# Kernel tuning notes

Measured on AMD Instinct MI355X. Metric: run time of the kernel, lower is better.

Reference implementation:

```python
import jax, jax.numpy as jnp
import numpy as np

B, S, D = 64, 2048, 512

def setup_inputs() -> dict:
    key = jax.random.key(0)
    k1, k2, k3, k4, k5 = jax.random.split(key, 5)
    x = jax.random.normal(k1, (B, S, D), dtype=jnp.float32)
    # torch Linear(dim, dim): weight [D, D], bias [D]
    W1 = jax.random.normal(k2, (D, D), dtype=jnp.float32) * (1.0 / np.sqrt(D))
    b1 = jax.random.normal(k3, (D,), dtype=jnp.float32) * 0.01
    # torch Linear(dim, 1): weight [1, D] -> stored as [D], bias scalar
    w2 = jax.random.normal(k4, (D,), dtype=jnp.float32) * (1.0 / np.sqrt(D))
    b2 = jax.random.normal(k5, (), dtype=jnp.float32) * 0.01
    return {"x": x, "W1": W1, "b1": b1, "w2": w2, "b2": b2}

def reference(x, W1, b1, w2, b2):
    # score MLP: Linear -> Tanh -> Linear(->1), squeeze
    h = jnp.tanh(jnp.einsum('bsd,ed->bse', x, W1) + b1)   # [B,S,D]
    scores = jnp.einsum('bsd,d->bs', h, w2) + b2          # [B,S]
    w = jax.nn.softmax(scores, axis=1)[..., None]         # [B,S,1]
    ctx = jnp.sum(x * w, axis=1)                          # [B,D]
    return (ctx, w)
```

## Files before the change

### kernel.cpp

```cpp
#include <hip/hip_runtime.h>
#include <hip/hip_bf16.h>

#define BB 64
#define SS 2048
#define DD 512
#define MTOT (BB * SS)

typedef __attribute__((ext_vector_type(8))) short short8;
typedef __attribute__((ext_vector_type(8))) unsigned short ushort8;
typedef __attribute__((ext_vector_type(4))) float f32x4;

__device__ __forceinline__ unsigned short f2bf(float f){
  union { float f; unsigned int u; } a; a.f = f;
  unsigned int r = a.u + 0x7fffu + ((a.u >> 16) & 1u);
  return (unsigned short)(r >> 16);
}

__device__ __forceinline__ ushort8 pack8(float4 a, float4 b){
  ushort8 u;
  u[0]=f2bf(a.x); u[1]=f2bf(a.y); u[2]=f2bf(a.z); u[3]=f2bf(a.w);
  u[4]=f2bf(b.x); u[5]=f2bf(b.y); u[6]=f2bf(b.z); u[7]=f2bf(b.w);
  return u;
}

__device__ __forceinline__ void gload_lds16(const unsigned short* g, unsigned short* l){
  __builtin_amdgcn_global_load_lds(
      (const __attribute__((address_space(1))) unsigned int*)g,
      (__attribute__((address_space(3))) unsigned int*)l, 16, 0, 0);
}

__global__ void cvt_w1_kernel(const float* __restrict__ W1, unsigned short* __restrict__ W1s){
  int i = blockIdx.x * blockDim.x + threadIdx.x;
  int s  = i >> 11;
  int g  = i & 2047;
  int kc = g >> 9;
  int e  = (g & 511) ^ kc;
  const float* src = W1 + (size_t)e * DD + s * 32 + kc * 8;
  float4 f0 = *(const float4*)src;
  float4 f1 = *(const float4*)(src + 4);
  *(ushort8*)(W1s + (size_t)i * 8) = pack8(f0, f1);
}

__launch_bounds__(512, 4)
__global__ void scores_kernel(const float* __restrict__ x,
                              const unsigned short* __restrict__ W1s,
                              const float* __restrict__ b1,
                              const float* __restrict__ w2,
                              float* __restrict__ scorep){
  __shared__ __align__(16) unsigned short lds[2][18432];

  const int t    = threadIdx.x;
  const int lane = t & 63;
  const int wid  = t >> 6;
  const int m0   = blockIdx.x * 64;
  const int arow = lane & 15;
  const int kgrp = lane >> 4;

  f32x4 acc[4][4];
  #pragma unroll
  for (int mt = 0; mt < 4; ++mt)
    #pragma unroll
    for (int et = 0; et < 4; ++et)
      acc[mt][et] = (f32x4){0.f, 0.f, 0.f, 0.f};

  const int srow = t >> 2;
  const int skc  = t & 3;
  const float* asrc0 = x + (size_t)(m0 + srow) * DD + skc * 8;
  const int awoff = ((skc << 6) + (srow ^ skc)) << 4;

  const unsigned short* bsrc0 = W1s + ((size_t)((wid << 2) << 6) + lane) * 8;

  #pragma unroll
  for (int j = 0; j < 4; ++j)
    gload_lds16(bsrc0 + j * 512, &lds[0][2048 + ((wid << 2) + j) * 512]);
  if (t < 256){
    float4 f0 = *(const float4*)asrc0;
    float4 f1 = *(const float4*)(asrc0 + 4);
    *(ushort8*)((char*)&lds[0][0] + awoff) = pack8(f0, f1);
  }
  __syncthreads();

  for (int s = 0; s < 16; ++s){
    unsigned short* cur = &lds[s & 1][0];
    unsigned short* nxt = &lds[(s + 1) & 1][0];

    float4 f0, f1;
    if (s < 15){
      const unsigned short* bs = bsrc0 + (size_t)(s + 1) * 16384;
      #pragma unroll
      for (int j = 0; j < 4; ++j)
        gload_lds16(bs + j * 512, nxt + 2048 + ((wid << 2) + j) * 512);
      if (t < 256){
        const float* as = asrc0 + (s + 1) * 32;
        f0 = *(const float4*)as;
        f1 = *(const float4*)(as + 4);
      }
    }

    short8 af[4], bf[4];
    #pragma unroll
    for (int mt = 0; mt < 4; ++mt){
      int row = mt * 16 + arow;
      af[mt] = *(const short8*)((char*)cur + (((kgrp << 6) + (row ^ kgrp)) << 4));
    }
    #pragma unroll
    for (int et = 0; et < 4; ++et){
      int e = (wid << 6) + (et << 4) + arow;
      bf[et] = *(const short8*)((char*)cur + 4096 + (((kgrp << 9) + (e ^ kgrp)) << 4));
    }

    __builtin_amdgcn_s_setprio(1);
    #pragma unroll
    for (int mt = 0; mt < 4; ++mt)
      #pragma unroll
      for (int et = 0; et < 4; ++et)
        acc[mt][et] = __builtin_amdgcn_mfma_f32_16x16x32_bf16(af[mt], bf[et], acc[mt][et], 0, 0, 0);
    __builtin_amdgcn_s_setprio(0);

    if (s < 15 && t < 256)
      *(ushort8*)((char*)nxt + awoff) = pack8(f0, f1);

    __syncthreads();
  }

  float ps[4][4];
  #pragma unroll
  for (int mt = 0; mt < 4; ++mt)
    #pragma unroll
    for (int i = 0; i < 4; ++i) ps[mt][i] = 0.f;

  #pragma unroll
  for (int et = 0; et < 4; ++et){
    int e = (wid << 6) + (et << 4) + arow;
    float b1v = b1[e];
    float w2v = w2[e];
    #pragma unroll
    for (int mt = 0; mt < 4; ++mt){
      #pragma unroll
      for (int i = 0; i < 4; ++i){
        float g = acc[mt][et][i] + b1v;
        g = fminf(15.f, fmaxf(-15.f, g));
        float ex = __expf(2.f * g);
        ps[mt][i] += (1.f - 2.f / (ex + 1.f)) * w2v;
      }
    }
  }
  #pragma unroll
  for (int mt = 0; mt < 4; ++mt)
    #pragma unroll
    for (int i = 0; i < 4; ++i){
      float v = ps[mt][i];
      v += __shfl_xor(v, 1);
      v += __shfl_xor(v, 2);
      v += __shfl_xor(v, 4);
      v += __shfl_xor(v, 8);
      ps[mt][i] = v;
    }
  float* psum = (float*)&lds[0][0];
  if ((lane & 15) == 0){
    #pragma unroll
    for (int mt = 0; mt < 4; ++mt)
      #pragma unroll
      for (int i = 0; i < 4; ++i)
        psum[wid * 64 + mt * 16 + (lane >> 4) * 4 + i] = ps[mt][i];
  }
  __syncthreads();
  if (t < 64){
    float ssum = 0.f;
    #pragma unroll
    for (int w = 0; w < 8; ++w) ssum += psum[w * 64 + t];
    scorep[m0 + t] = ssum;
  }
}

__global__ void softmax_kernel(const float* __restrict__ scorep, float* __restrict__ wout){
  const int b = blockIdx.x;
  const int t = threadIdx.x;
  float v[8];
  #pragma unroll
  for (int i = 0; i < 8; ++i) v[i] = scorep[(size_t)b * SS + t + i * 256];
  float m = v[0];
  #pragma unroll
  for (int i = 1; i < 8; ++i) m = fmaxf(m, v[i]);
  #pragma unroll
  for (int msk = 32; msk >= 1; msk >>= 1) m = fmaxf(m, __shfl_xor(m, msk));
  __shared__ float redm[4], reds[4];
  if ((t & 63) == 0) redm[t >> 6] = m;
  __syncthreads();
  m = fmaxf(fmaxf(redm[0], redm[1]), fmaxf(redm[2], redm[3]));
  float s = 0.f;
  #pragma unroll
  for (int i = 0; i < 8; ++i){ v[i] = __expf(v[i] - m); s += v[i]; }
  #pragma unroll
  for (int msk = 32; msk >= 1; msk >>= 1) s += __shfl_xor(s, msk);
  if ((t & 63) == 0) reds[t >> 6] = s;
  __syncthreads();
  s = reds[0] + reds[1] + reds[2] + reds[3];
  float inv = 1.f / s;
  #pragma unroll
  for (int i = 0; i < 8; ++i) wout[(size_t)b * SS + t + i * 256] = v[i] * inv;
}

__global__ void ctx_partial_kernel(const float* __restrict__ x, const float* __restrict__ wout,
                                   float* __restrict__ ctxp){
  __shared__ float red[4][512];
  const int t   = threadIdx.x;
  const int sub = t >> 7;
  const int dt  = t & 127;
  const int b   = blockIdx.x >> 3;
  const int sc  = blockIdx.x & 7;
  const float* xb = x + (size_t)b * SS * DD;
  const int s0 = sc * 256 + sub * 64;
  float4 acc = {0.f, 0.f, 0.f, 0.f};
  for (int s = s0; s < s0 + 64; ++s){
    float wv = wout[(size_t)b * SS + s];
    float4 xv = *(const float4*)(xb + (size_t)s * DD + dt * 4);
    acc.x += wv * xv.x; acc.y += wv * xv.y; acc.z += wv * xv.z; acc.w += wv * xv.w;
  }
  *(float4*)&red[sub][dt * 4] = acc;
  __syncthreads();
  if (t < 128){
    float4 r0 = *(const float4*)&red[0][t * 4];
    float4 r1 = *(const float4*)&red[1][t * 4];
    float4 r2 = *(const float4*)&red[2][t * 4];
    float4 r3 = *(const float4*)&red[3][t * 4];
    float4 o = { r0.x+r1.x+r2.x+r3.x, r0.y+r1.y+r2.y+r3.y,
                 r0.z+r1.z+r2.z+r3.z, r0.w+r1.w+r2.w+r3.w };
    *(float4*)&ctxp[((size_t)(b * 8 + sc)) * DD + t * 4] = o;
  }
}

__global__ void ctx_reduce_kernel(const float* __restrict__ ctxp, float* __restrict__ ctx){
  int i = blockIdx.x * blockDim.x + threadIdx.x;
  int b = i >> 9;
  int d = i & 511;
  float s = 0.f;
  #pragma unroll
  for (int sc = 0; sc < 8; ++sc) s += ctxp[((size_t)(b * 8 + sc)) * DD + d];
  ctx[(size_t)b * DD + d] = s;
}

extern "C" void kernel_launch(void* const* d_in, const int* in_sizes, int n_in,
                              void* d_out, int out_size, void* d_ws, size_t ws_size,
                              hipStream_t stream){
  const float* x  = (const float*)d_in[0];
  const float* W1 = (const float*)d_in[1];
  const float* b1 = (const float*)d_in[2];
  const float* w2 = (const float*)d_in[3];

  float* ctx  = (float*)d_out;
  float* wout = (float*)d_out + BB * DD;

  unsigned short* W1s = (unsigned short*)d_ws;
  float* scorep = (float*)((char*)d_ws + (512u << 10));
  float* ctxp   = (float*)d_ws;

  hipLaunchKernelGGL(cvt_w1_kernel,      dim3(128),  dim3(256), 0, stream, W1, W1s);
  hipLaunchKernelGGL(scores_kernel,      dim3(2048), dim3(512), 0, stream, x, W1s, b1, w2, scorep);
  hipLaunchKernelGGL(softmax_kernel,     dim3(64),   dim3(256), 0, stream, scorep, wout);
  hipLaunchKernelGGL(ctx_partial_kernel, dim3(512),  dim3(512), 0, stream, x, wout, ctxp);
  hipLaunchKernelGGL(ctx_reduce_kernel,  dim3(128),  dim3(256), 0, stream, ctxp, ctx);
}
```

Measured before the change: 163.0 us.

## Write bf16 copy of x in scores kernel and read it for context sum

The scores kernel now writes its bf16-converted x tiles out to a workspace buffer. The context weighted-sum kernel then reads that half-size copy instead of the fp32 x, so the second pass moves half the bytes. In exchange the first pass pays an extra 128 MB write, and the context sum loses precision because x is rounded to bf16. The path runs only when the workspace is large enough; the x prefetch is also moved ahead of the W1 loads.

```diff
diff --git a/kernel.cpp b/kernel.cpp
--- a/kernel.cpp
+++ b/kernel.cpp
@@ -11,9 +11,13 @@
 typedef __attribute__((ext_vector_type(4))) float f32x4;
 
 __device__ __forceinline__ unsigned short f2bf(float f){
-  union { float f; unsigned int u; } a; a.f = f;
-  unsigned int r = a.u + 0x7fffu + ((a.u >> 16) & 1u);
-  return (unsigned short)(r >> 16);
+  __hip_bfloat16 h = __float2bfloat16(f);
+  return *reinterpret_cast<unsigned short*>(&h);
+}
+
+__device__ __forceinline__ float bf2f(unsigned short u){
+  union { unsigned int i; float f; } a; a.i = ((unsigned int)u) << 16;
+  return a.f;
 }
 
 __device__ __forceinline__ ushort8 pack8(float4 a, float4 b){
@@ -46,7 +50,8 @@
                               const unsigned short* __restrict__ W1s,
                               const float* __restrict__ b1,
                               const float* __restrict__ w2,
-                              float* __restrict__ scorep){
+                              float* __restrict__ scorep,
+                              unsigned short* __restrict__ xbf){
   __shared__ __align__(16) unsigned short lds[2][18432];
 
   const int t    = threadIdx.x;
@@ -66,17 +71,23 @@
   const int srow = t >> 2;
   const int skc  = t & 3;
   const float* asrc0 = x + (size_t)(m0 + srow) * DD + skc * 8;
+  unsigned short* xdst0 = xbf ? xbf + (size_t)(m0 + srow) * DD + skc * 8 : nullptr;
   const int awoff = ((skc << 6) + (srow ^ skc)) << 4;
 
   const unsigned short* bsrc0 = W1s + ((size_t)((wid << 2) << 6) + lane) * 8;
 
+  float4 pf0, pf1;
+  if (t < 256){
+    pf0 = *(const float4*)asrc0;
+    pf1 = *(const float4*)(asrc0 + 4);
+  }
   #pragma unroll
   for (int j = 0; j < 4; ++j)
     gload_lds16(bsrc0 + j * 512, &lds[0][2048 + ((wid << 2) + j) * 512]);
   if (t < 256){
-    float4 f0 = *(const float4*)asrc0;
-    float4 f1 = *(const float4*)(asrc0 + 4);
-    *(ushort8*)((char*)&lds[0][0] + awoff) = pack8(f0, f1);
+    ushort8 u = pack8(pf0, pf1);
+    *(ushort8*)((char*)&lds[0][0] + awoff) = u;
+    if (xdst0) *(ushort8*)xdst0 = u;
   }
   __syncthreads();
 
@@ -86,15 +97,15 @@
 
     float4 f0, f1;
     if (s < 15){
-      const unsigned short* bs = bsrc0 + (size_t)(s + 1) * 16384;
-      #pragma unroll
-      for (int j = 0; j < 4; ++j)
-        gload_lds16(bs + j * 512, nxt + 2048 + ((wid << 2) + j) * 512);
       if (t < 256){
         const float* as = asrc0 + (s + 1) * 32;
         f0 = *(const float4*)as;
         f1 = *(const float4*)(as + 4);
       }
+      const unsigned short* bs = bsrc0 + (size_t)(s + 1) * 16384;
+      #pragma unroll
+      for (int j = 0; j < 4; ++j)
+        gload_lds16(bs + j * 512, nxt + 2048 + ((wid << 2) + j) * 512);
     }
 
     short8 af[4], bf[4];
@@ -117,9 +128,11 @@
         acc[mt][et] = __builtin_amdgcn_mfma_f32_16x16x32_bf16(af[mt], bf[et], acc[mt][et], 0, 0, 0);
     __builtin_amdgcn_s_setprio(0);
 
-    if (s < 15 && t < 256)
-      *(ushort8*)((char*)nxt + awoff) = pack8(f0, f1);
-
+    if (s < 15 && t < 256){
+      ushort8 u = pack8(f0, f1);
+      *(ushort8*)((char*)nxt + awoff) = u;
+      if (xdst0) *(ushort8*)(xdst0 + (s + 1) * 32) = u;
+    }
     __syncthreads();
   }
 
@@ -199,6 +212,40 @@
   float inv = 1.f / s;
   #pragma unroll
   for (int i = 0; i < 8; ++i) wout[(size_t)b * SS + t + i * 256] = v[i] * inv;
+}
+
+__global__ void ctx_partial_bf16_kernel(const unsigned short* __restrict__ xbf,
+                                        const float* __restrict__ wout,
+                                        float* __restrict__ ctxp){
+  __shared__ float red[8][512];
+  const int t   = threadIdx.x;
+  const int sub = t >> 6;
+  const int dt  = t & 63;
+  const int b   = blockIdx.x >> 3;
+  const int sc  = blockIdx.x & 7;
+  const unsigned short* xb = xbf + (size_t)b * SS * DD + dt * 8;
+  const int s0 = sc * 256 + sub * 32;
+  float a[8];
+  #pragma unroll
+  for (int j = 0; j < 8; ++j) a[j] = 0.f;
+  for (int s = s0; s < s0 + 32; ++s){
+    float wv = wout[(size_t)b * SS + s];
+    ushort8 xv = *(const ushort8*)(xb + (size_t)s * DD);
+    #pragma unroll
+    for (int j = 0; j < 8; ++j) a[j] += wv * bf2f(xv[j]);
+  }
+  #pragma unroll
+  for (int j = 0; j < 8; ++j) red[sub][dt * 8 + j] = a[j];
+  __syncthreads();
+  if (t < 128){
+    float4 o = {0.f, 0.f, 0.f, 0.f};
+    #pragma unroll
+    for (int sb = 0; sb < 8; ++sb){
+      float4 r = *(const float4*)&red[sb][t * 4];
+      o.x += r.x; o.y += r.y; o.z += r.z; o.w += r.w;
+    }
+    *(float4*)&ctxp[((size_t)(b * 8 + sc)) * DD + t * 4] = o;
+  }
 }
 
 __global__ void ctx_partial_kernel(const float* __restrict__ x, const float* __restrict__ wout,
@@ -253,11 +300,24 @@
 
   unsigned short* W1s = (unsigned short*)d_ws;
   float* scorep = (float*)((char*)d_ws + (512u << 10));
-  float* ctxp   = (float*)d_ws;
-
-  hipLaunchKernelGGL(cvt_w1_kernel,      dim3(128),  dim3(256), 0, stream, W1, W1s);
-  hipLaunchKernelGGL(scores_kernel,      dim3(2048), dim3(512), 0, stream, x, W1s, b1, w2, scorep);
-  hipLaunchKernelGGL(softmax_kernel,     dim3(64),   dim3(256), 0, stream, scorep, wout);
-  hipLaunchKernelGGL(ctx_partial_kernel, dim3(512),  dim3(512), 0, stream, x, wout, ctxp);
-  hipLaunchKernelGGL(ctx_reduce_kernel,  dim3(128),  dim3(256), 0, stream, ctxp, ctx);
-}
+  const size_t xbf_bytes = (size_t)MTOT * DD * 2;
+  const size_t need = (1u << 20) + xbf_bytes + (1u << 20);
+  bool use_bf16x = (ws_size >= need);
+
+  hipLaunchKernelGGL(cvt_w1_kernel, dim3(128), dim3(256), 0, stream, W1, W1s);
+
+  if (use_bf16x){
+    unsigned short* xbf = (unsigned short*)((char*)d_ws + (1u << 20));
+    float* ctxp = (float*)((char*)d_ws + (1u << 20) + xbf_bytes);
+    hipLaunchKernelGGL(scores_kernel,          dim3(2048), dim3(512), 0, stream, x, W1s, b1, w2, scorep, xbf);
+    hipLaunchKernelGGL(softmax_kernel,         dim3(64),   dim3(256), 0, stream, scorep, wout);
+    hipLaunchKernelGGL(ctx_partial_bf16_kernel,dim3(512),  dim3(512), 0, stream, xbf, wout, ctxp);
+    hipLaunchKernelGGL(ctx_reduce_kernel,      dim3(128),  dim3(256), 0, stream, ctxp, ctx);
+  } else {
+    float* ctxp = (float*)d_ws;
+    hipLaunchKernelGGL(scores_kernel,          dim3(2048), dim3(512), 0, stream, x, W1s, b1, w2, scorep, (unsigned short*)nullptr);
+    hipLaunchKernelGGL(softmax_kernel,         dim3(64),   dim3(256), 0, stream, scorep, wout);
+    hipLaunchKernelGGL(ctx_partial_kernel,     dim3(512),  dim3(512), 0, stream, x, wout, ctxp);
+    hipLaunchKernelGGL(ctx_reduce_kernel,      dim3(128),  dim3(256), 0, stream, ctxp, ctx);
+  }
+}
```

Measured after the change: 210.7 us. 1.29x slower.

## Load GEMM operands directly from global memory into registers, dropping LDS staging

Applied to the files above, without the earlier changes.

The scores GEMM no longer stages the x and W1 tiles through double-buffered shared memory. Each lane now loads its MFMA fragments straight from global memory (x as fp32 converted in registers, W1 as row-major bf16), and a loose barrier every two k-steps keeps waves roughly in step so they share cache. W1 conversion becomes a plain row-major cast, and the float-to-bf16 routine now uses the library intrinsic. This removes LDS traffic and per-step block syncs, but each of the 8 waves re-reads the same x rows from L1/L2, so global and cache traffic goes up and there is no explicit prefetch.

```diff
diff --git a/kernel.cpp b/kernel.cpp
--- a/kernel.cpp
+++ b/kernel.cpp
@@ -10,44 +10,33 @@
 typedef __attribute__((ext_vector_type(8))) unsigned short ushort8;
 typedef __attribute__((ext_vector_type(4))) float f32x4;
 
-__device__ __forceinline__ unsigned short f2bf(float f){
-  union { float f; unsigned int u; } a; a.f = f;
-  unsigned int r = a.u + 0x7fffu + ((a.u >> 16) & 1u);
-  return (unsigned short)(r >> 16);
-}
-
-__device__ __forceinline__ ushort8 pack8(float4 a, float4 b){
-  ushort8 u;
+__device__ __forceinline__ short f2bf(float f){
+  __hip_bfloat16 h = __float2bfloat16(f);
+  return *reinterpret_cast<short*>(&h);
+}
+
+__device__ __forceinline__ short8 pack8(float4 a, float4 b){
+  short8 u;
   u[0]=f2bf(a.x); u[1]=f2bf(a.y); u[2]=f2bf(a.z); u[3]=f2bf(a.w);
   u[4]=f2bf(b.x); u[5]=f2bf(b.y); u[6]=f2bf(b.z); u[7]=f2bf(b.w);
   return u;
 }
 
-__device__ __forceinline__ void gload_lds16(const unsigned short* g, unsigned short* l){
-  __builtin_amdgcn_global_load_lds(
-      (const __attribute__((address_space(1))) unsigned int*)g,
-      (__attribute__((address_space(3))) unsigned int*)l, 16, 0, 0);
-}
-
-__global__ void cvt_w1_kernel(const float* __restrict__ W1, unsigned short* __restrict__ W1s){
+__global__ void cvt_w1_kernel(const float* __restrict__ W1, unsigned short* __restrict__ W1b){
   int i = blockIdx.x * blockDim.x + threadIdx.x;
-  int s  = i >> 11;
-  int g  = i & 2047;
-  int kc = g >> 9;
-  int e  = (g & 511) ^ kc;
-  const float* src = W1 + (size_t)e * DD + s * 32 + kc * 8;
+  const float* src = W1 + (size_t)i * 8;
   float4 f0 = *(const float4*)src;
   float4 f1 = *(const float4*)(src + 4);
-  *(ushort8*)(W1s + (size_t)i * 8) = pack8(f0, f1);
+  *(short8*)(W1b + (size_t)i * 8) = pack8(f0, f1);
 }
 
 __launch_bounds__(512, 4)
 __global__ void scores_kernel(const float* __restrict__ x,
-                              const unsigned short* __restrict__ W1s,
+                              const unsigned short* __restrict__ W1b,
                               const float* __restrict__ b1,
                               const float* __restrict__ w2,
                               float* __restrict__ scorep){
-  __shared__ __align__(16) unsigned short lds[2][18432];
+  __shared__ float psum[8 * 64];
 
   const int t    = threadIdx.x;
   const int lane = t & 63;
@@ -63,64 +52,39 @@
     for (int et = 0; et < 4; ++et)
       acc[mt][et] = (f32x4){0.f, 0.f, 0.f, 0.f};
 
-  const int srow = t >> 2;
-  const int skc  = t & 3;
-  const float* asrc0 = x + (size_t)(m0 + srow) * DD + skc * 8;
-  const int awoff = ((skc << 6) + (srow ^ skc)) << 4;
-
-  const unsigned short* bsrc0 = W1s + ((size_t)((wid << 2) << 6) + lane) * 8;
-
-  #pragma unroll
-  for (int j = 0; j < 4; ++j)
-    gload_lds16(bsrc0 + j * 512, &lds[0][2048 + ((wid << 2) + j) * 512]);
-  if (t < 256){
-    float4 f0 = *(const float4*)asrc0;
-    float4 f1 = *(const float4*)(asrc0 + 4);
-    *(ushort8*)((char*)&lds[0][0] + awoff) = pack8(f0, f1);
-  }
-  __syncthreads();
-
+  const float* ab0 = x + (size_t)(m0 +  0 + arow) * DD + kgrp * 8;
+  const float* ab1 = x + (size_t)(m0 + 16 + arow) * DD + kgrp * 8;
+  const float* ab2 = x + (size_t)(m0 + 32 + arow) * DD + kgrp * 8;
+  const float* ab3 = x + (size_t)(m0 + 48 + arow) * DD + kgrp * 8;
+  const int e0 = (wid << 6) + arow;
+  const unsigned short* bb0 = W1b + (size_t)(e0 +  0) * DD + kgrp * 8;
+  const unsigned short* bb1 = W1b + (size_t)(e0 + 16) * DD + kgrp * 8;
+  const unsigned short* bb2 = W1b + (size_t)(e0 + 32) * DD + kgrp * 8;
+  const unsigned short* bb3 = W1b + (size_t)(e0 + 48) * DD + kgrp * 8;
+
+  #pragma unroll
   for (int s = 0; s < 16; ++s){
-    unsigned short* cur = &lds[s & 1][0];
-    unsigned short* nxt = &lds[(s + 1) & 1][0];
-
-    float4 f0, f1;
-    if (s < 15){
-      const unsigned short* bs = bsrc0 + (size_t)(s + 1) * 16384;
-      #pragma unroll
-      for (int j = 0; j < 4; ++j)
-        gload_lds16(bs + j * 512, nxt + 2048 + ((wid << 2) + j) * 512);
-      if (t < 256){
-        const float* as = asrc0 + (s + 1) * 32;
-        f0 = *(const float4*)as;
-        f1 = *(const float4*)(as + 4);
-      }
+    const int ao = s * 32;
+    short8 af[4], bf[4];
+    {
+      float4 f0, f1;
+      f0 = *(const float4*)(ab0 + ao); f1 = *(const float4*)(ab0 + ao + 4); af[0] = pack8(f0, f1);
+      f0 = *(const float4*)(ab1 + ao); f1 = *(const float4*)(ab1 + ao + 4); af[1] = pack8(f0, f1);
+      f0 = *(const float4*)(ab2 + ao); f1 = *(const float4*)(ab2 + ao + 4); af[2] = pack8(f0, f1);
+      f0 = *(const float4*)(ab3 + ao); f1 = *(const float4*)(ab3 + ao + 4); af[3] = pack8(f0, f1);
     }
-
-    short8 af[4], bf[4];
-    #pragma unroll
-    for (int mt = 0; mt < 4; ++mt){
-      int row = mt * 16 + arow;
-      af[mt] = *(const short8*)((char*)cur + (((kgrp << 6) + (row ^ kgrp)) << 4));
-    }
-    #pragma unroll
-    for (int et = 0; et < 4; ++et){
-      int e = (wid << 6) + (et << 4) + arow;
-      bf[et] = *(const short8*)((char*)cur + 4096 + (((kgrp << 9) + (e ^ kgrp)) << 4));
-    }
-
-    __builtin_amdgcn_s_setprio(1);
+    bf[0] = *(const short8*)(bb0 + ao);
+    bf[1] = *(const short8*)(bb1 + ao);
+    bf[2] = *(const short8*)(bb2 + ao);
+    bf[3] = *(const short8*)(bb3 + ao);
+
     #pragma unroll
     for (int mt = 0; mt < 4; ++mt)
       #pragma unroll
       for (int et = 0; et < 4; ++et)
         acc[mt][et] = __builtin_amdgcn_mfma_f32_16x16x32_bf16(af[mt], bf[et], acc[mt][et], 0, 0, 0);
-    __builtin_amdgcn_s_setprio(0);
-
-    if (s < 15 && t < 256)
-      *(ushort8*)((char*)nxt + awoff) = pack8(f0, f1);
-
-    __syncthreads();
+
+    if ((s & 1) == 1 && s < 15) __builtin_amdgcn_s_barrier();
   }
 
   float ps[4][4];
@@ -156,7 +120,6 @@
       v += __shfl_xor(v, 8);
       ps[mt][i] = v;
     }
-  float* psum = (float*)&lds[0][0];
   if ((lane & 15) == 0){
     #pragma unroll
     for (int mt = 0; mt < 4; ++mt)
@@ -251,12 +214,12 @@
   float* ctx  = (float*)d_out;
   float* wout = (float*)d_out + BB * DD;
 
-  unsigned short* W1s = (unsigned short*)d_ws;
+  unsigned short* W1b = (unsigned short*)d_ws;
   float* scorep = (float*)((char*)d_ws + (512u << 10));
   float* ctxp   = (float*)d_ws;
 
-  hipLaunchKernelGGL(cvt_w1_kernel,      dim3(128),  dim3(256), 0, stream, W1, W1s);
-  hipLaunchKernelGGL(scores_kernel,      dim3(2048), dim3(512), 0, stream, x, W1s, b1, w2, scorep);
+  hipLaunchKernelGGL(cvt_w1_kernel,      dim3(128),  dim3(256), 0, stream, W1, W1b);
+  hipLaunchKernelGGL(scores_kernel,      dim3(2048), dim3(512), 0, stream, x, W1b, b1, w2, scorep);
   hipLaunchKernelGGL(softmax_kernel,     dim3(64),   dim3(256), 0, stream, scorep, wout);
   hipLaunchKernelGGL(ctx_partial_kernel, dim3(512),  dim3(512), 0, stream, x, wout, ctxp);
   hipLaunchKernelGGL(ctx_reduce_kernel,  dim3(128),  dim3(256), 0, stream, ctxp, ctx);
```

Result: slower. 416.8 us (+155.8%).

## Fuse softmax and context reduction into scores GEMM with online-softmax partials

Applied to the files above, without the earlier changes.

The scores kernel now keeps the whole 64x512 bf16 x tile resident in LDS. After computing the 64 scores it also computes a per-block max, exp-sum and weighted context partial from that resident tile. A single merge kernel combines the 32 partials per batch and writes both the normalized weights and ctx. This removes the second full fp32 read of x and two kernel launches. The costs are more LDS per block (occupancy drops to 2 blocks), the context being computed from bf16-rounded x, and a reworked pipeline with manual waitcnt and barriers for x prefetch.

```diff
diff --git a/kernel.cpp b/kernel.cpp
--- a/kernel.cpp
+++ b/kernel.cpp
@@ -7,22 +7,28 @@
 #define MTOT (BB * SS)
 
 typedef __attribute__((ext_vector_type(8))) short short8;
-typedef __attribute__((ext_vector_type(8))) unsigned short ushort8;
+typedef __attribute__((ext_vector_type(4))) short s16x4;
 typedef __attribute__((ext_vector_type(4))) float f32x4;
 
-__device__ __forceinline__ unsigned short f2bf(float f){
-  union { float f; unsigned int u; } a; a.f = f;
-  unsigned int r = a.u + 0x7fffu + ((a.u >> 16) & 1u);
-  return (unsigned short)(r >> 16);
-}
-
-__device__ __forceinline__ ushort8 pack8(float4 a, float4 b){
-  ushort8 u;
+__device__ __forceinline__ short f2bf(float f){
+  __hip_bfloat16 h = __float2bfloat16(f);
+  return *reinterpret_cast<short*>(&h);
+}
+__device__ __forceinline__ float bf2f(unsigned short u){
+  union { unsigned int i; float f; } a; a.i = ((unsigned int)u) << 16;
+  return a.f;
+}
+__device__ __forceinline__ short8 pack8(float4 a, float4 b){
+  short8 u;
   u[0]=f2bf(a.x); u[1]=f2bf(a.y); u[2]=f2bf(a.z); u[3]=f2bf(a.w);
   u[4]=f2bf(b.x); u[5]=f2bf(b.y); u[6]=f2bf(b.z); u[7]=f2bf(b.w);
   return u;
 }
-
+__device__ __forceinline__ s16x4 pack4(float4 a){
+  s16x4 u;
+  u[0]=f2bf(a.x); u[1]=f2bf(a.y); u[2]=f2bf(a.z); u[3]=f2bf(a.w);
+  return u;
+}
 __device__ __forceinline__ void gload_lds16(const unsigned short* g, unsigned short* l){
   __builtin_amdgcn_global_load_lds(
       (const __attribute__((address_space(1))) unsigned int*)g,
@@ -38,16 +44,22 @@
   const float* src = W1 + (size_t)e * DD + s * 32 + kc * 8;
   float4 f0 = *(const float4*)src;
   float4 f1 = *(const float4*)(src + 4);
-  *(ushort8*)(W1s + (size_t)i * 8) = pack8(f0, f1);
-}
-
-__launch_bounds__(512, 4)
+  *(short8*)(W1s + (size_t)i * 8) = pack8(f0, f1);
+}
+
+__launch_bounds__(512, 2)
 __global__ void scores_kernel(const float* __restrict__ x,
                               const unsigned short* __restrict__ W1s,
                               const float* __restrict__ b1,
                               const float* __restrict__ w2,
-                              float* __restrict__ scorep){
-  __shared__ __align__(16) unsigned short lds[2][18432];
+                              float* __restrict__ scorep,
+                              float* __restrict__ mpart,
+                              float* __restrict__ spart,
+                              float* __restrict__ ctxp){
+  __shared__ __align__(16) unsigned short Atile[64 * 512];
+  __shared__ __align__(16) unsigned short Bbuf[2][16384];
+  __shared__ float psum[8 * 64];
+  __shared__ float pbuf[64];
 
   const int t    = threadIdx.x;
   const int lane = t & 63;
@@ -63,50 +75,53 @@
     for (int et = 0; et < 4; ++et)
       acc[mt][et] = (f32x4){0.f, 0.f, 0.f, 0.f};
 
-  const int srow = t >> 2;
-  const int skc  = t & 3;
-  const float* asrc0 = x + (size_t)(m0 + srow) * DD + skc * 8;
-  const int awoff = ((skc << 6) + (srow ^ skc)) << 4;
-
-  const unsigned short* bsrc0 = W1s + ((size_t)((wid << 2) << 6) + lane) * 8;
+  const int ar  = t >> 3;
+  const int aq  = t & 7;
+  const int arx = ar & 7;
+  const float* asrc = x + (size_t)(m0 + ar) * DD + aq * 4;
+
+  const unsigned short* bsrc = W1s + ((size_t)(wid << 8) + lane) * 8;
+
+  float4 a_pre[2];
 
   #pragma unroll
   for (int j = 0; j < 4; ++j)
-    gload_lds16(bsrc0 + j * 512, &lds[0][2048 + ((wid << 2) + j) * 512]);
-  if (t < 256){
-    float4 f0 = *(const float4*)asrc0;
-    float4 f1 = *(const float4*)(asrc0 + 4);
-    *(ushort8*)((char*)&lds[0][0] + awoff) = pack8(f0, f1);
-  }
-  __syncthreads();
-
+    gload_lds16(bsrc + j * 512, &Bbuf[0][((wid << 2) + j) * 512]);
+  float4 a0 = *(const float4*)asrc;
+  #pragma unroll
+  for (int j = 0; j < 4; ++j)
+    gload_lds16(bsrc + 16384 + j * 512, &Bbuf[1][((wid << 2) + j) * 512]);
+  a_pre[1] = *(const float4*)(asrc + 32);
+  {
+    s16x4 u = pack4(a0);
+    *(s16x4*)((char*)Atile + ((ar * 64 + ((aq >> 1) ^ arx)) << 4) + (aq & 1) * 8) = u;
+  }
+  asm volatile("s_waitcnt vmcnt(5)" ::: "memory");
+  asm volatile("s_waitcnt lgkmcnt(0)" ::: "memory");
+  __builtin_amdgcn_s_barrier();
+  __builtin_amdgcn_sched_barrier(0);
+
+  #pragma unroll
   for (int s = 0; s < 16; ++s){
-    unsigned short* cur = &lds[s & 1][0];
-    unsigned short* nxt = &lds[(s + 1) & 1][0];
-
-    float4 f0, f1;
-    if (s < 15){
-      const unsigned short* bs = bsrc0 + (size_t)(s + 1) * 16384;
+    if (s >= 1 && s < 15){
+      const unsigned short* bs = bsrc + (size_t)(s + 1) * 16384;
       #pragma unroll
       for (int j = 0; j < 4; ++j)
-        gload_lds16(bs + j * 512, nxt + 2048 + ((wid << 2) + j) * 512);
-      if (t < 256){
-        const float* as = asrc0 + (s + 1) * 32;
-        f0 = *(const float4*)as;
-        f1 = *(const float4*)(as + 4);
-      }
-    }
+        gload_lds16(bs + j * 512, &Bbuf[(s + 1) & 1][((wid << 2) + j) * 512]);
+    }
+    if (s < 14)
+      a_pre[s & 1] = *(const float4*)(asrc + (s + 2) * 32);
 
     short8 af[4], bf[4];
     #pragma unroll
     for (int mt = 0; mt < 4; ++mt){
       int row = mt * 16 + arow;
-      af[mt] = *(const short8*)((char*)cur + (((kgrp << 6) + (row ^ kgrp)) << 4));
+      af[mt] = *(const short8*)((char*)Atile + ((row * 64 + ((s * 4 + kgrp) ^ (row & 7))) << 4));
     }
     #pragma unroll
     for (int et = 0; et < 4; ++et){
       int e = (wid << 6) + (et << 4) + arow;
-      bf[et] = *(const short8*)((char*)cur + 4096 + (((kgrp << 9) + (e ^ kgrp)) << 4));
+      bf[et] = *(const short8*)((char*)&Bbuf[s & 1][0] + (((kgrp << 9) + (e ^ kgrp)) << 4));
     }
 
     __builtin_amdgcn_s_setprio(1);
@@ -117,10 +132,18 @@
         acc[mt][et] = __builtin_amdgcn_mfma_f32_16x16x32_bf16(af[mt], bf[et], acc[mt][et], 0, 0, 0);
     __builtin_amdgcn_s_setprio(0);
 
-    if (s < 15 && t < 256)
-      *(ushort8*)((char*)nxt + awoff) = pack8(f0, f1);
-
-    __syncthreads();
+    if (s < 15){
+      s16x4 u = pack4(a_pre[(s + 1) & 1]);
+      *(s16x4*)((char*)Atile + ((ar * 64 + (((s + 1) * 4 + (aq >> 1)) ^ arx)) << 4) + (aq & 1) * 8) = u;
+    }
+
+    if (s < 15){
+      if (s < 14) asm volatile("s_waitcnt vmcnt(1)" ::: "memory");
+      else        asm volatile("s_waitcnt vmcnt(0)" ::: "memory");
+      asm volatile("s_waitcnt lgkmcnt(0)" ::: "memory");
+      __builtin_amdgcn_s_barrier();
+      __builtin_amdgcn_sched_barrier(0);
+    }
   }
 
   float ps[4][4];
@@ -156,7 +179,6 @@
       v += __shfl_xor(v, 8);
       ps[mt][i] = v;
     }
-  float* psum = (float*)&lds[0][0];
   if ((lane & 15) == 0){
     #pragma unroll
     for (int mt = 0; mt < 4; ++mt)
@@ -165,79 +187,63 @@
         psum[wid * 64 + mt * 16 + (lane >> 4) * 4 + i] = ps[mt][i];
   }
   __syncthreads();
+
   if (t < 64){
-    float ssum = 0.f;
-    #pragma unroll
-    for (int w = 0; w < 8; ++w) ssum += psum[w * 64 + t];
-    scorep[m0 + t] = ssum;
-  }
-}
-
-__global__ void softmax_kernel(const float* __restrict__ scorep, float* __restrict__ wout){
+    float score = 0.f;
+    #pragma unroll
+    for (int w = 0; w < 8; ++w) score += psum[w * 64 + t];
+    scorep[m0 + t] = score;
+    float m = score;
+    #pragma unroll
+    for (int msk = 32; msk >= 1; msk >>= 1) m = fmaxf(m, __shfl_xor(m, msk));
+    float p = __expf(score - m);
+    float sg = p;
+    #pragma unroll
+    for (int msk = 32; msk >= 1; msk >>= 1) sg += __shfl_xor(sg, msk);
+    if (t == 0){ mpart[blockIdx.x] = m; spart[blockIdx.x] = sg; }
+    pbuf[t] = p;
+  }
+  __syncthreads();
+
+  {
+    float a = 0.f;
+    const int cg = (t >> 3);
+    const int ch = (t & 7) * 2;
+    #pragma unroll 8
+    for (int r = 0; r < 64; ++r){
+      float pw = pbuf[r];
+      unsigned short uxv = *(const unsigned short*)((char*)Atile + ((r * 64 + (cg ^ (r & 7))) << 4) + ch);
+      a += pw * bf2f(uxv);
+    }
+    ctxp[(size_t)blockIdx.x * DD + t] = a;
+  }
+}
+
+__global__ void merge_kernel(const float* __restrict__ scorep,
+                             const float* __restrict__ mpart,
+                             const float* __restrict__ spart,
+                             const float* __restrict__ ctxp,
+                             float* __restrict__ ctx,
+                             float* __restrict__ wout){
   const int b = blockIdx.x;
   const int t = threadIdx.x;
-  float v[8];
-  #pragma unroll
-  for (int i = 0; i < 8; ++i) v[i] = scorep[(size_t)b * SS + t + i * 256];
-  float m = v[0];
-  #pragma unroll
-  for (int i = 1; i < 8; ++i) m = fmaxf(m, v[i]);
-  #pragma unroll
-  for (int msk = 32; msk >= 1; msk >>= 1) m = fmaxf(m, __shfl_xor(m, msk));
-  __shared__ float redm[4], reds[4];
-  if ((t & 63) == 0) redm[t >> 6] = m;
-  __syncthreads();
-  m = fmaxf(fmaxf(redm[0], redm[1]), fmaxf(redm[2], redm[3]));
-  float s = 0.f;
-  #pragma unroll
-  for (int i = 0; i < 8; ++i){ v[i] = __expf(v[i] - m); s += v[i]; }
-  #pragma unroll
-  for (int msk = 32; msk >= 1; msk >>= 1) s += __shfl_xor(s, msk);
-  if ((t & 63) == 0) reds[t >> 6] = s;
-  __syncthreads();
-  s = reds[0] + reds[1] + reds[2] + reds[3];
-  float inv = 1.f / s;
-  #pragma unroll
-  for (int i = 0; i < 8; ++i) wout[(size_t)b * SS + t + i * 256] = v[i] * inv;
-}
-
-__global__ void ctx_partial_kernel(const float* __restrict__ x, const float* __restrict__ wout,
-                                   float* __restrict__ ctxp){
-  __shared__ float red[4][512];
-  const int t   = threadIdx.x;
-  const int sub = t >> 7;
-  const int dt  = t & 127;
-  const int b   = blockIdx.x >> 3;
-  const int sc  = blockIdx.x & 7;
-  const float* xb = x + (size_t)b * SS * DD;
-  const int s0 = sc * 256 + sub * 64;
-  float4 acc = {0.f, 0.f, 0.f, 0.f};
-  for (int s = s0; s < s0 + 64; ++s){
-    float wv = wout[(size_t)b * SS + s];
-    float4 xv = *(const float4*)(xb + (size_t)s * DD + dt * 4);
-    acc.x += wv * xv.x; acc.y += wv * xv.y; acc.z += wv * xv.z; acc.w += wv * xv.w;
-  }
-  *(float4*)&red[sub][dt * 4] = acc;
-  __syncthreads();
-  if (t < 128){
-    float4 r0 = *(const float4*)&red[0][t * 4];
-    float4 r1 = *(const float4*)&red[1][t * 4];
-    float4 r2 = *(const float4*)&red[2][t * 4];
-    float4 r3 = *(const float4*)&red[3][t * 4];
-    float4 o = { r0.x+r1.x+r2.x+r3.x, r0.y+r1.y+r2.y+r3.y,
-                 r0.z+r1.z+r2.z+r3.z, r0.w+r1.w+r2.w+r3.w };
-    *(float4*)&ctxp[((size_t)(b * 8 + sc)) * DD + t * 4] = o;
-  }
-}
-
-__global__ void ctx_reduce_kernel(const float* __restrict__ ctxp, float* __restrict__ ctx){
-  int i = blockIdx.x * blockDim.x + threadIdx.x;
-  int b = i >> 9;
-  int d = i & 511;
-  float s = 0.f;
-  #pragma unroll
-  for (int sc = 0; sc < 8; ++sc) s += ctxp[((size_t)(b * 8 + sc)) * DD + d];
-  ctx[(size_t)b * DD + d] = s;
+  float M = -1e30f;
+  #pragma unroll
+  for (int i = 0; i < 32; ++i) M = fmaxf(M, mpart[b * 32 + i]);
+  float Z = 0.f;
+  #pragma unroll
+  for (int i = 0; i < 32; ++i) Z += spart[b * 32 + i] * __expf(mpart[b * 32 + i] - M);
+  float invZ = 1.f / Z;
+  float a = 0.f;
+  #pragma unroll
+  for (int i = 0; i < 32; ++i)
+    a += __expf(mpart[b * 32 + i] - M) * ctxp[(size_t)(b * 32 + i) * DD + t];
+  ctx[(size_t)b * DD + t] = a * invZ;
+  #pragma unroll
+  for (int j = 0; j < 4; ++j){
+    int s = j * 512 + t;
+    wout[(size_t)b * SS + s] = __expf(scorep[(size_t)b * SS + s] - M) * invZ;
+  }
 }
 
 extern "C" void kernel_launch(void* const* d_in, const int* in_sizes, int n_in,
@@ -251,13 +257,16 @@
   float* ctx  = (float*)d_out;
   float* wout = (float*)d_out + BB * DD;
 
-  unsigned short* W1s = (unsigned short*)d_ws;
-  float* scorep = (float*)((char*)d_ws + (512u << 10));
-  float* ctxp   = (float*)d_ws;
-
-  hipLaunchKernelGGL(cvt_w1_kernel,      dim3(128),  dim3(256), 0, stream, W1, W1s);
-  hipLaunchKernelGGL(scores_kernel,      dim3(2048), dim3(512), 0, stream, x, W1s, b1, w2, scorep);
-  hipLaunchKernelGGL(softmax_kernel,     dim3(64),   dim3(256), 0, stream, scorep, wout);
-  hipLaunchKernelGGL(ctx_partial_kernel, dim3(512),  dim3(512), 0, stream, x, wout, ctxp);
-  hipLaunchKernelGGL(ctx_reduce_kernel,  dim3(128),  dim3(256), 0, stream, ctxp, ctx);
-}
+  char* ws = (char*)d_ws;
+  unsigned short* W1s = (unsigned short*)ws;
+  float* scorep = (float*)(ws + (512u << 10));
+  float* mpart  = (float*)(ws + (1024u << 10));
+  float* spart  = (float*)(ws + (1024u << 10) + (8u << 10));
+  float* ctxp   = (float*)(ws + (1024u << 10) + (16u << 10));
+
+  hipLaunchKernelGGL(cvt_w1_kernel, dim3(128),  dim3(256), 0, stream, W1, W1s);
+  hipLaunchKernelGGL(scores_kernel, dim3(2048), dim3(512), 0, stream,
+                     x, W1s, b1, w2, scorep, mpart, spart, ctxp);
+  hipLaunchKernelGGL(merge_kernel,  dim3(64),   dim3(512), 0, stream,
+                     scorep, mpart, spart, ctxp, ctx, wout);
+}
```

Measured after the change: 207.4 us. 27.3% more time.
